# Optimization experiments

Hardware: AMD Instinct MI355X
Metric: run time of the kernel (lower is better)

## Reference

```python
import jax, jax.numpy as jnp
import numpy as np
from jax import lax

FEAT_STRIDE = 16
PRE_NMS_TOP_N = 6000   # cfg['TEST'].RPN_PRE_NMS_TOP_N
POST_NMS_TOP_N = 300   # cfg['TEST'].RPN_POST_NMS_TOP_N
NMS_THRESH = 0.7       # cfg['TEST'].RPN_NMS_THRESH
MIN_SIZE = 16.0        # cfg['TEST'].RPN_MIN_SIZE
B, A, H, W = 32, 9, 128, 128
NEG_INF = jnp.float32(-1e30)


def _whctrs(a):
    w = a[2] - a[0] + 1.0
    h = a[3] - a[1] + 1.0
    return w, h, a[0] + 0.5 * (w - 1), a[1] + 0.5 * (h - 1)

def _mkanchors(ws, hs, xc, yc):
    ws = ws[:, None]; hs = hs[:, None]
    return np.hstack((xc - 0.5 * (ws - 1), yc - 0.5 * (hs - 1),
                      xc + 0.5 * (ws - 1), yc + 0.5 * (hs - 1)))

def _ratio_enum(anchor, ratios):
    w, h, xc, yc = _whctrs(anchor)
    size = w * h
    ws = np.round(np.sqrt(size / ratios))
    hs = np.round(ws * ratios)
    return _mkanchors(ws, hs, xc, yc)

def _scale_enum(anchor, scales):
    w, h, xc, yc = _whctrs(anchor)
    return _mkanchors(w * scales, h * scales, xc, yc)

def generate_anchors(base_size=16, ratios=np.array([0.5, 1.0, 2.0]), scales=np.array([8.0, 16.0, 32.0])):
    base = np.array([1, 1, base_size, base_size], dtype=np.float64) - 1
    ra = _ratio_enum(base, ratios)
    return np.vstack([_scale_enum(ra[i], scales) for i in range(ra.shape[0])]).astype(np.float32)

_BASE_ANCHORS = generate_anchors()  # (A, 4)

def _all_anchors(h, w):
    sx = np.arange(w) * FEAT_STRIDE
    sy = np.arange(h) * FEAT_STRIDE
    sx, sy = np.meshgrid(sx, sy)  # row-major (h, w) matches permute(0,2,3,1) ordering
    shifts = np.stack([sx.ravel(), sy.ravel(), sx.ravel(), sy.ravel()], axis=1).astype(np.float32)
    return jnp.asarray((shifts[:, None, :] + _BASE_ANCHORS[None, :, :]).reshape(-1, 4))  # (h*w*A, 4)

# ---- bbox_transform_inv / clip_boxes ----

def _decode(anchors, deltas):
    ws = anchors[:, 2] - anchors[:, 0] + 1.0
    hs = anchors[:, 3] - anchors[:, 1] + 1.0
    cx = anchors[:, 0] + 0.5 * ws
    cy = anchors[:, 1] + 0.5 * hs
    dx, dy, dw, dh = deltas[:, 0], deltas[:, 1], deltas[:, 2], deltas[:, 3]
    pcx = dx * ws + cx
    pcy = dy * hs + cy
    pw = jnp.exp(dw) * ws
    ph = jnp.exp(dh) * hs
    return jnp.stack([pcx - 0.5 * pw, pcy - 0.5 * ph, pcx + 0.5 * pw, pcy + 0.5 * ph], axis=1)

def _clip(b, imh, imw):
    x1 = jnp.clip(b[:, 0], 0.0, imw - 1.0)
    y1 = jnp.clip(b[:, 1], 0.0, imh - 1.0)
    x2 = jnp.clip(b[:, 2], 0.0, imw - 1.0)
    y2 = jnp.clip(b[:, 3], 0.0, imh - 1.0)
    return jnp.stack([x1, y1, x2, y2], axis=1)

# ---- greedy NMS: pick top-score box, suppress IoU > thresh, repeat POST times ----

def _nms_select(boxes, scores):
    # boxes: (PRE, 4) score-sorted; scores: (PRE,)
    areas = (boxes[:, 2] - boxes[:, 0] + 1.0) * (boxes[:, 3] - boxes[:, 1] + 1.0)

    def body(i, st):
        s, keep, valid = st
        j = jnp.argmax(s)
        keep = keep.at[i].set(j)
        valid = valid.at[i].set(s[j] > NEG_INF)
        b = boxes[j]
        xx1 = jnp.maximum(b[0], boxes[:, 0])
        yy1 = jnp.maximum(b[1], boxes[:, 1])
        xx2 = jnp.minimum(b[2], boxes[:, 2])
        yy2 = jnp.minimum(b[3], boxes[:, 3])
        inter = jnp.maximum(xx2 - xx1 + 1.0, 0.0) * jnp.maximum(yy2 - yy1 + 1.0, 0.0)
        iou = inter / jnp.maximum(areas[j] + areas - inter, 1e-6)
        s = jnp.where(iou > NMS_THRESH, NEG_INF, s)  # suppresses j itself (IoU = 1)
        return s, keep, valid

    init = (scores, jnp.zeros((POST_NMS_TOP_N,), jnp.int32), jnp.zeros((POST_NMS_TOP_N,), bool))
    _, keep, valid = lax.fori_loop(0, POST_NMS_TOP_N, body, init)
    return keep, valid

def _per_image(sc, dl, info, anchors):
    prop = _clip(_decode(anchors, dl), info[0], info[1])  # (K*A, 4)
    ws = prop[:, 2] - prop[:, 0] + 1.0
    hs = prop[:, 3] - prop[:, 1] + 1.0
    min_sz = MIN_SIZE * info[2]
    sc = jnp.where((ws >= min_sz) & (hs >= min_sz), sc, NEG_INF)
    top_s, top_i = lax.top_k(sc, PRE_NMS_TOP_N)
    cand = prop[top_i]  # (PRE, 4)
    keep, valid = _nms_select(cand, top_s)
    return cand[keep] * valid[:, None].astype(cand.dtype)  # zero-pad invalid rows

def _forward(rpn_cls_prob, rpn_bbox_pred, im_info):
    b, _, h, w = rpn_cls_prob.shape
    anchors = _all_anchors(h, w)
    scores = rpn_cls_prob[:, A:, :, :].transpose(0, 2, 3, 1).reshape(b, -1)  # (b, h*w*A)
    deltas = rpn_bbox_pred.transpose(0, 2, 3, 1).reshape(b, -1, 4)           # (b, h*w*A, 4)
    boxes = jax.vmap(lambda s, d, i: _per_image(s, d, i, anchors))(scores, deltas, im_info)
    ids = jnp.broadcast_to(jnp.arange(b, dtype=boxes.dtype)[:, None, None], (b, POST_NMS_TOP_N, 1))
    return jnp.concatenate([ids, boxes], axis=2)  # (b, POST, 5): [batch_idx, x1, y1, x2, y2]

def setup_inputs() -> dict:
    key = jax.random.key(0)
    k1, k2 = jax.random.split(key)
    rpn_cls_prob = jax.random.uniform(k1, (B, 2 * A, H, W), dtype=jnp.float32)
    rpn_bbox_pred = jax.random.normal(k2, (B, 4 * A, H, W), dtype=jnp.float32) * 0.2
    im_info = jnp.tile(jnp.array([[H * FEAT_STRIDE, W * FEAT_STRIDE, 1.0]], dtype=jnp.float32), (B, 1))
    return {"rpn_cls_prob": rpn_cls_prob, "rpn_bbox_pred": rpn_bbox_pred, "im_info": im_info}

def reference(rpn_cls_prob, rpn_bbox_pred, im_info):
    return _forward(rpn_cls_prob, rpn_bbox_pred, im_info)
```

## Files before the change

kernel.cpp:

```cpp
#include <hip/hip_runtime.h>
#include <cstdint>
#include <cstddef>

#pragma clang fp contract(off)

typedef unsigned long long u64;

#define NB 32
#define NA 9
#define NH 128
#define NW 128
#define HW (NH*NW)
#define NANCH (NA*HW)
#define PRE_N 6000
#define POST_N 300
#define CAND_CAP 8192
#define NMS_T 0.7f
#define GX_GATHER 24
#define NBOX 6144
#define CH 512

__constant__ float c_wa[9] = {184.f,368.f,736.f,128.f,256.f,512.f,88.f,176.f,352.f};
__constant__ float c_ha[9] = {96.f,192.f,384.f,128.f,256.f,512.f,176.f,352.f,704.f};

__device__ __forceinline__ float4 decode_clip(int a, int h, int w,
    float dx, float dy, float dlw, float dlh, float imh, float imw) {
  float wa = c_wa[a], ha = c_ha[a];
  float cx = (float)w * 16.0f + 8.0f;
  float cy = (float)h * 16.0f + 8.0f;
  float pcx = dx * wa + cx;
  float pcy = dy * ha + cy;
  float pw = expf(dlw) * wa;
  float ph = expf(dlh) * ha;
  float x1 = pcx - 0.5f * pw;
  float y1 = pcy - 0.5f * ph;
  float x2 = pcx + 0.5f * pw;
  float y2 = pcy + 0.5f * ph;
  float4 r;
  r.x = fminf(fmaxf(x1, 0.0f), imw - 1.0f);
  r.y = fminf(fmaxf(y1, 0.0f), imh - 1.0f);
  r.z = fminf(fmaxf(x2, 0.0f), imw - 1.0f);
  r.w = fminf(fmaxf(y2, 0.0f), imh - 1.0f);
  return r;
}

__device__ __forceinline__ unsigned score_key(float sc, float bw, float bh, float msz) {
  unsigned bits = __float_as_uint(sc);
  unsigned key = (bits & 0x80000000u) ? ~bits : (bits | 0x80000000u);
  if (!(bw >= msz && bh >= msz)) key = 0u;
  return key;
}

__device__ __forceinline__ bool sup_test4(float4 v, float ar, float4 p, float pa) {
  float xx1 = fmaxf(p.x, v.x), yy1 = fmaxf(p.y, v.y);
  float xx2 = fminf(p.z, v.z), yy2 = fminf(p.w, v.w);
  float iw = fmaxf(xx2 - xx1 + 1.0f, 0.0f);
  float ih = fmaxf(yy2 - yy1 + 1.0f, 0.0f);
  float inter = iw * ih;
  float iou = inter / fmaxf(pa + ar - inter, 1e-6f);
  return iou > NMS_T;
}

__device__ __forceinline__ u64 shfl_xor_u64(u64 x, int m) {
  int lo = __shfl_xor((int)(unsigned)x, m, 64);
  int hi = __shfl_xor((int)(unsigned)(x >> 32), m, 64);
  return ((u64)(unsigned)hi << 32) | (unsigned)lo;
}

__device__ __forceinline__ void reg_step(u64 v[8], int t, int k, int j) {
  #pragma unroll
  for (int r = 0; r < 8; ++r) {
    if ((r & j) == 0) {
      int e = (t << 3) + r;
      bool up = ((e & k) == 0);
      u64 x = v[r], y = v[r | j];
      u64 mx = x > y ? x : y, mn = x > y ? y : x;
      v[r]     = up ? mx : mn;
      v[r | j] = up ? mn : mx;
    }
  }
}

__device__ __forceinline__ void shfl_step(u64 v[8], int t, int k, int j) {
  int m = j >> 3;
  bool lower = ((t & m) == 0);
  #pragma unroll
  for (int r = 0; r < 8; ++r) {
    int e = (t << 3) + r;
    bool up = ((e & k) == 0);
    u64 pv = shfl_xor_u64(v[r], m);
    bool keepmax = (up == lower);
    u64 x = v[r];
    u64 mx = x > pv ? x : pv, mn = x > pv ? pv : x;
    v[r] = keepmax ? mx : mn;
  }
}

__device__ __forceinline__ void lds_step(u64* sm, u64 v[8], int t, int k, int j) {
  int m = j >> 3;
  __syncthreads();
  #pragma unroll
  for (int r = 0; r < 8; ++r) sm[(r << 10) | t] = v[r];
  __syncthreads();
  bool lower = ((t & m) == 0);
  bool up = (((t << 3) & k) == 0);
  bool keepmax = (up == lower);
  int pt = t ^ m;
  #pragma unroll
  for (int r = 0; r < 8; ++r) {
    u64 pv = sm[(r << 10) | pt];
    u64 x = v[r];
    u64 mx = x > pv ? x : pv, mn = x > pv ? pv : x;
    v[r] = keepmax ? mx : mn;
  }
}

__device__ void find_B(const unsigned* __restrict__ hb, unsigned* part,
                       unsigned* outB, unsigned* outCum) {
  int tid = threadIdx.x;
  unsigned s = 0;
  for (int i = 0; i < 16; ++i) s += hb[tid*16 + i];
  part[tid] = s;
  __syncthreads();
  for (int off = 1; off < 256; off <<= 1) {
    unsigned v = (tid + off < 256) ? part[tid + off] : 0u;
    __syncthreads();
    part[tid] += v;
    __syncthreads();
  }
  unsigned St = part[tid];
  unsigned Sn = (tid < 255) ? part[tid + 1] : 0u;
  if (St >= (unsigned)PRE_N && Sn < (unsigned)PRE_N) {
    unsigned cum = Sn, B = 0, cumAbove = Sn;
    for (int i = 15; i >= 0; --i) {
      unsigned v = hb[tid*16 + i];
      if (cum + v >= (unsigned)PRE_N) { B = (unsigned)(tid*16 + i); cumAbove = cum; break; }
      cum += v;
    }
    *outB = B; *outCum = cumAbove;
  }
  __syncthreads();
}

__device__ void find_thr(const unsigned* __restrict__ hb2, unsigned B, unsigned cum0,
                         unsigned* part, unsigned* outThr) {
  int tid = threadIdx.x;
  unsigned s = 0;
  for (int i = 0; i < 16; ++i) s += hb2[tid*16 + i];
  part[tid] = s;
  __syncthreads();
  for (int off = 1; off < 256; off <<= 1) {
    unsigned v = (tid + off < 256) ? part[tid + off] : 0u;
    __syncthreads();
    part[tid] += v;
    __syncthreads();
  }
  unsigned St = cum0 + part[tid];
  unsigned Sn = cum0 + ((tid < 255) ? part[tid + 1] : 0u);
  if (St >= (unsigned)PRE_N && Sn < (unsigned)PRE_N) {
    unsigned cum = Sn, t = 1u;
    for (int i = 15; i >= 0; --i) {
      unsigned v = hb2[tid*16 + i];
      if (cum + v >= (unsigned)PRE_N) {
        t = (B << 20) | ((unsigned)(tid*16 + i) << 8);
        break;
      }
      cum += v;
    }
    if (t == 0u) t = 1u;
    *outThr = t;
  }
  __syncthreads();
}

__global__ __launch_bounds__(256) void k_keys(const float* __restrict__ cls,
    const float* __restrict__ dl, const float* __restrict__ info,
    unsigned* __restrict__ keys, unsigned* __restrict__ hist) {
  __shared__ unsigned hsh[4096];
  int tid = threadIdx.x;
  for (int i = tid; i < 4096; i += 256) hsh[i] = 0;
  int t = blockIdx.x * 256 + tid;
  int b = blockIdx.y;
  int hw0 = t * 4;
  int h = hw0 >> 7;
  const float* dlb  = dl  + (size_t)b * (4*NA*HW);
  const float* clsb = cls + (size_t)b * (2*NA*HW);
  float imh = info[b*3+0], imw = info[b*3+1];
  float msz = 16.0f * info[b*3+2];
  unsigned* kb = keys + (size_t)b * NANCH;
  __syncthreads();
  #pragma unroll
  for (int a = 0; a < 9; ++a) {
    float4 dx4 = *(const float4*)&dlb[(a*4+0)*HW + hw0];
    float4 dy4 = *(const float4*)&dlb[(a*4+1)*HW + hw0];
    float4 dw4 = *(const float4*)&dlb[(a*4+2)*HW + hw0];
    float4 dh4 = *(const float4*)&dlb[(a*4+3)*HW + hw0];
    float4 sc4 = *(const float4*)&clsb[(NA+a)*HW + hw0];
    uint4 out;
    {
      float4 bx = decode_clip(a, h, (hw0+0)&127, dx4.x, dy4.x, dw4.x, dh4.x, imh, imw);
      out.x = score_key(sc4.x, bx.z-bx.x+1.0f, bx.w-bx.y+1.0f, msz);
    }
    {
      float4 bx = decode_clip(a, h, (hw0+1)&127, dx4.y, dy4.y, dw4.y, dh4.y, imh, imw);
      out.y = score_key(sc4.y, bx.z-bx.x+1.0f, bx.w-bx.y+1.0f, msz);
    }
    {
      float4 bx = decode_clip(a, h, (hw0+2)&127, dx4.z, dy4.z, dw4.z, dh4.z, imh, imw);
      out.z = score_key(sc4.z, bx.z-bx.x+1.0f, bx.w-bx.y+1.0f, msz);
    }
    {
      float4 bx = decode_clip(a, h, (hw0+3)&127, dx4.w, dy4.w, dw4.w, dh4.w, imh, imw);
      out.w = score_key(sc4.w, bx.z-bx.x+1.0f, bx.w-bx.y+1.0f, msz);
    }
    *(uint4*)&kb[a*HW + hw0] = out;
    atomicAdd(&hsh[out.x >> 20], 1u);
    atomicAdd(&hsh[out.y >> 20], 1u);
    atomicAdd(&hsh[out.z >> 20], 1u);
    atomicAdd(&hsh[out.w >> 20], 1u);
  }
  __syncthreads();
  unsigned* gb = hist + ((size_t)b << 12);
  for (int i = tid; i < 4096; i += 256) {
    unsigned v = hsh[i];
    if (v) atomicAdd(&gb[i], v);
  }
}

__global__ __launch_bounds__(256) void k_hist2(const unsigned* __restrict__ keys,
    const unsigned* __restrict__ hist1, unsigned* __restrict__ hist2) {
  __shared__ unsigned h[4096];
  __shared__ unsigned part[256];
  __shared__ unsigned sB, sCum;
  int b = blockIdx.y, tid = threadIdx.x;
  for (int i = tid; i < 4096; i += 256) h[i] = 0;
  __syncthreads();
  find_B(hist1 + ((size_t)b << 12), part, &sB, &sCum);
  unsigned B = sB;
  const unsigned* kb = keys + (size_t)b * NANCH;
  for (int i = blockIdx.x * 256 + tid; i < NANCH; i += gridDim.x * 256) {
    unsigned k = kb[i];
    if ((k >> 20) == B) atomicAdd(&h[(k >> 8) & 4095u], 1u);
  }
  __syncthreads();
  unsigned* gb = hist2 + ((size_t)b << 12);
  for (int i = tid; i < 4096; i += 256) { unsigned v = h[i]; if (v) atomicAdd(&gb[i], v); }
}

__global__ __launch_bounds__(256) void k_gather(const unsigned* __restrict__ keys,
    const unsigned* __restrict__ hist1, const unsigned* __restrict__ hist2,
    const float* __restrict__ dl, const float* __restrict__ info,
    unsigned* __restrict__ cnt, u64* __restrict__ cand,
    float4* __restrict__ boxes) {
  int b = blockIdx.y, tid = threadIdx.x;
  int lane = tid & 63, wv = tid >> 6;
  __shared__ unsigned part[256];
  __shared__ unsigned sB, sCum, sThr;
  __shared__ unsigned wcnt[4], woff[4], blkbase;
  if (tid == 0) sThr = 1u;
  __syncthreads();
  find_B(hist1 + ((size_t)b << 12), part, &sB, &sCum);
  find_thr(hist2 + ((size_t)b << 12), sB, sCum, part, &sThr);
  unsigned t_ = sThr;
  const unsigned* kb = keys + (size_t)b * NANCH;
  const float* dlb = dl + (size_t)b * (4*NA*HW);
  float imh = info[b*3+0], imw = info[b*3+1];
  u64* cb = cand + (size_t)b * CAND_CAP;
  float4* bxc = boxes + (size_t)b * CAND_CAP;
  unsigned* cp = cnt + (size_t)b * 64;
  const int PER_BLK = NANCH / GX_GATHER;
  int base0 = blockIdx.x * PER_BLK;
  for (int it = 0; it < PER_BLK / 256; ++it) {
    int j = base0 + it * 256 + tid;
    unsigned key = kb[j];
    bool pass = key >= t_;
    u64 mask = __ballot(pass);
    if (lane == 0) wcnt[wv] = (unsigned)__popcll(mask);
    __syncthreads();
    if (tid == 0) {
      unsigned s0 = 0;
      for (int w = 0; w < 4; ++w) { woff[w] = s0; s0 += wcnt[w]; }
      blkbase = s0 ? atomicAdd(cp, s0) : 0u;
    }
    __syncthreads();
    if (pass) {
      unsigned pos = blkbase + woff[wv] + (unsigned)__popcll(mask & ((1ull << lane) - 1ull));
      if (pos < CAND_CAP) {
        int a = j >> 14, hw = j & (HW - 1);
        unsigned oi = (unsigned)(hw * 9 + a);
        unsigned noi = (~oi) & 0x3FFFFu;
        cb[pos] = ((u64)key << 32) | ((u64)noi << 13) | (u64)pos;
        bxc[pos] = decode_clip(a, hw >> 7, hw & 127,
                               dlb[(a*4+0)*HW + hw], dlb[(a*4+1)*HW + hw],
                               dlb[(a*4+2)*HW + hw], dlb[(a*4+3)*HW + hw],
                               imh, imw);
      }
    }
    __syncthreads();
  }
}

__global__ __launch_bounds__(1024) void k_final4(const u64* __restrict__ cand,
    const unsigned* __restrict__ cnt, const float4* __restrict__ boxes,
    float* __restrict__ out) {
  __shared__ float4 bx[NBOX];
  __shared__ float4 cbox2[CH];
  __shared__ float  carea2[CH];
  __shared__ float4 kbox[POST_N];
  __shared__ float  karea[POST_N];
  __shared__ unsigned supf[CH];
  __shared__ u64 sup[CH][9];
  __shared__ u64 aliveM[8];
  __shared__ u64 kgW[8];
  __shared__ int s_nk;
  u64* sm = (u64*)bx;

  int b = blockIdx.x, tid = threadIdx.x;
  int lane = tid & 63;
  if (tid == 0) s_nk = 0;

  unsigned effcnt = cnt[b * 64];
  if (effcnt > CAND_CAP) effcnt = CAND_CAP;
  const u64* cb = cand + (size_t)b * CAND_CAP;
  int e0 = tid << 3;
  u64 v[8];
  #pragma unroll
  for (int r = 0; r < 8; ++r)
    v[r] = ((unsigned)(e0 + r) < effcnt) ? cb[e0 + r] : 0ull;

  for (int k = 2; k <= 8; k <<= 1)
    for (int j = k >> 1; j >= 1; j >>= 1) reg_step(v, tid, k, j);
  for (int k = 16; k <= CAND_CAP; k <<= 1) {
    int j = k >> 1;
    for (; j >= 512; j >>= 1) lds_step(sm, v, tid, k, j);
    for (; j >= 8;   j >>= 1) shfl_step(v, tid, k, j);
    for (; j >= 1;   j >>= 1) reg_step(v, tid, k, j);
  }
  __syncthreads();

  const float4* bxc = boxes + (size_t)b * CAND_CAP;
  #pragma unroll
  for (int r = 0; r < 8; ++r) {
    int rank = e0 + r;
    if (rank < NBOX) {
      u64 ck = (rank < PRE_N) ? v[r] : 0ull;
      float4 w = make_float4(0.f, 0.f, -1.f, -1.f);
      if ((unsigned)(ck >> 32) != 0u)
        w = bxc[(unsigned)(ck & 0x1FFFu)];
      bx[rank] = w;
    }
  }
  __syncthreads();

  float* ob = out + (size_t)b * (POST_N * 5);
  int c = tid & (CH - 1);
  int seg = tid >> 9;

  for (int base = 0; base < NBOX; base += CH) {
    if (tid < CH) {
      float4 w = bx[base + tid];
      supf[tid] = (w.z - w.x + 1.0f > 0.0f) ? 0u : 1u;
    }
    __syncthreads();
    int nk0 = s_nk;

    if (supf[c] == 0u && nk0 > 0) {
      float4 w = bx[base + c];
      float ar = (w.z - w.x + 1.0f) * (w.w - w.y + 1.0f);
      bool dead = false;
      for (int k = seg; k < nk0; k += 2) {
        if (sup_test4(w, ar, kbox[k], karea[k])) { dead = true; break; }
      }
      if (dead) supf[c] = 1u;
    }
    __syncthreads();

    if (tid < CH) {
      u64 am = __ballot(supf[tid] == 0u);
      if (lane == 0) aliveM[tid >> 6] = am;
    }
    __syncthreads();

    int na = 0;
    #pragma unroll
    for (int g = 0; g < 8; ++g) na += (int)__popcll(aliveM[g]);
    if (na == 0) continue;

    if (tid < CH && supf[tid] == 0u) {
      int cg2 = tid >> 6;
      int pre = 0;
      #pragma unroll
      for (int g = 0; g < 8; ++g) if (g < cg2) pre += (int)__popcll(aliveM[g]);
      pre += (int)__popcll(aliveM[cg2] & ((1ull << (tid & 63)) - 1ull));
      float4 w = bx[base + tid];
      cbox2[pre] = w;
      carea2[pre] = (w.z - w.x + 1.0f) * (w.w - w.y + 1.0f);
    }
    __syncthreads();

    {
      int i = c;
      if (i < na) {
        int ngi = (i >> 6) + 1;
        int gA = seg ? (ngi >> 1) : 0;
        int gB = seg ? ngi : (ngi >> 1);
        if (gA < gB) {
          float4 vi = cbox2[i];
          float ai = carea2[i];
          for (int g = gA; g < gB; ++g) {
            int jmax = i - (g << 6);
            if (jmax > 64) jmax = 64;
            u64 r = 0;
            #pragma unroll 4
            for (int j = 0; j < jmax; ++j) {
              if (sup_test4(vi, ai, cbox2[(g << 6) + j], carea2[(g << 6) + j]))
                r |= 1ull << j;
            }
            sup[i][g] = r;
          }
        }
      }
    }
    __syncthreads();

    if (tid < 64) {
      u64 kw[8];
      #pragma unroll
      for (int s = 0; s < 8; ++s) {
        u64 kg = 0;
        if (s * 64 < na) {
          int cc = s * 64 + lane;
          bool a = (cc < na);
          #pragma unroll
          for (int g = 0; g < 8; ++g) {
            if (g < s && a) a = (sup[cc][g] & kw[g]) == 0ull;
          }
          u64 r = a ? sup[cc][s] : 0ull;
          u64 cm = __ballot(a);
          while (cm) {
            int j = __builtin_ctzll(cm);
            kg |= 1ull << j;
            u64 rem = __ballot((r >> j) & 1ull);
            cm &= ~(rem | (1ull << j));
          }
        }
        kw[s] = kg;
      }
      if (lane == 0) {
        #pragma unroll
        for (int s = 0; s < 8; ++s) kgW[s] = kw[s];
      }
    }
    __syncthreads();

    if (tid < na) {
      int s = tid >> 6;
      u64 kgw = kgW[s];
      bool kept = (kgw >> (tid & 63)) & 1;
      int pre = 0;
      #pragma unroll
      for (int g = 0; g < 8; ++g) if (g < s) pre += (int)__popcll(kgW[g]);
      pre += (int)__popcll(kgw & ((1ull << (tid & 63)) - 1ull));
      int rank = nk0 + pre;
      if (kept && rank < POST_N) {
        float4 w = cbox2[tid];
        kbox[rank] = w; karea[rank] = carea2[tid];
        ob[rank*5+0] = (float)b;
        ob[rank*5+1] = w.x; ob[rank*5+2] = w.y; ob[rank*5+3] = w.z; ob[rank*5+4] = w.w;
      }
    }
    if (tid == 0) {
      int tot = 0;
      #pragma unroll
      for (int s = 0; s < 8; ++s) tot += (int)__popcll(kgW[s]);
      int nn = nk0 + tot;
      s_nk = nn < POST_N ? nn : POST_N;
    }
    __syncthreads();
    if (s_nk >= POST_N) break;
  }
  __syncthreads();
  int nk = s_nk;
  for (int r = nk + tid; r < POST_N; r += 1024) {
    ob[r*5+0] = (float)b;
    ob[r*5+1] = 0.f; ob[r*5+2] = 0.f; ob[r*5+3] = 0.f; ob[r*5+4] = 0.f;
  }
}

extern "C" void kernel_launch(void* const* d_in, const int* in_sizes, int n_in,
                              void* d_out, int out_size, void* d_ws, size_t ws_size,
                              hipStream_t stream) {
  const float* cls  = (const float*)d_in[0];
  const float* dl   = (const float*)d_in[1];
  const float* info = (const float*)d_in[2];
  float* out = (float*)d_out;
  char* ws = (char*)d_ws;

  const size_t OFF_KEYS = 0;
  const size_t OFF_H1   = 18874368;
  const size_t OFF_H2   = 19398656;
  const size_t OFF_CNT  = 19922944;
  const size_t OFF_CAND = 19931136;
  const size_t OFF_BOX  = 22028288;
  const size_t WS_NEED  = 26222592;
  if (ws_size < WS_NEED) return;

  unsigned* keys  = (unsigned*)(ws + OFF_KEYS);
  unsigned* h1    = (unsigned*)(ws + OFF_H1);
  unsigned* h2    = (unsigned*)(ws + OFF_H2);
  unsigned* cnt   = (unsigned*)(ws + OFF_CNT);
  u64* cand = (u64*)(ws + OFF_CAND);
  float4* boxes = (float4*)(ws + OFF_BOX);

  hipMemsetAsync(ws + OFF_H1, 0, OFF_CAND - OFF_H1, stream);

  dim3 g1(HW / 1024, NB);
  k_keys<<<g1, 256, 0, stream>>>(cls, dl, info, keys, h1);
  dim3 gh(8, NB);
  k_hist2<<<gh, 256, 0, stream>>>(keys, h1, h2);
  dim3 gg(GX_GATHER, NB);
  k_gather<<<gg, 256, 0, stream>>>(keys, h1, h2, dl, info, cnt, cand, boxes);
  k_final4<<<NB, 1024, 0, stream>>>(cand, cnt, boxes, out);
}
```

Baseline: 332.4 us.

## Fuse second-level histogram and gather into one per-image select kernel

Merges k_hist2 and k_gather into a single 1024-thread block per image. The block builds the refinement histogram in shared memory, computes the threshold locally, and compacts candidates with a two-pass count-then-write scheme using per-wave offsets, which removes the global atomics and the per-iteration block barriers. The NMS keep-scan in k_final4 now prefetches the suppression rows into registers. This cuts a kernel launch and a memset range but reduces parallelism to 32 blocks for the key scans, which each read the key array twice.

```diff
diff --git a/kernel.cpp b/kernel.cpp
--- a/kernel.cpp
+++ b/kernel.cpp
@@ -16,7 +16,6 @@
 #define POST_N 300
 #define CAND_CAP 8192
 #define NMS_T 0.7f
-#define GX_GATHER 24
 #define NBOX 6144
 #define CH 512
 
@@ -118,26 +117,31 @@
 __device__ void find_B(const unsigned* __restrict__ hb, unsigned* part,
                        unsigned* outB, unsigned* outCum) {
   int tid = threadIdx.x;
-  unsigned s = 0;
-  for (int i = 0; i < 16; ++i) s += hb[tid*16 + i];
-  part[tid] = s;
+  if (tid < 256) {
+    unsigned s = 0;
+    for (int i = 0; i < 16; ++i) s += hb[tid*16 + i];
+    part[tid] = s;
+  }
   __syncthreads();
   for (int off = 1; off < 256; off <<= 1) {
-    unsigned v = (tid + off < 256) ? part[tid + off] : 0u;
-    __syncthreads();
-    part[tid] += v;
-    __syncthreads();
-  }
-  unsigned St = part[tid];
-  unsigned Sn = (tid < 255) ? part[tid + 1] : 0u;
-  if (St >= (unsigned)PRE_N && Sn < (unsigned)PRE_N) {
-    unsigned cum = Sn, B = 0, cumAbove = Sn;
-    for (int i = 15; i >= 0; --i) {
-      unsigned v = hb[tid*16 + i];
-      if (cum + v >= (unsigned)PRE_N) { B = (unsigned)(tid*16 + i); cumAbove = cum; break; }
-      cum += v;
-    }
-    *outB = B; *outCum = cumAbove;
+    unsigned v = 0;
+    if (tid < 256 && tid + off < 256) v = part[tid + off];
+    __syncthreads();
+    if (tid < 256) part[tid] += v;
+    __syncthreads();
+  }
+  if (tid < 256) {
+    unsigned St = part[tid];
+    unsigned Sn = (tid < 255) ? part[tid + 1] : 0u;
+    if (St >= (unsigned)PRE_N && Sn < (unsigned)PRE_N) {
+      unsigned cum = Sn, B = 0, cumAbove = Sn;
+      for (int i = 15; i >= 0; --i) {
+        unsigned v = hb[tid*16 + i];
+        if (cum + v >= (unsigned)PRE_N) { B = (unsigned)(tid*16 + i); cumAbove = cum; break; }
+        cum += v;
+      }
+      *outB = B; *outCum = cumAbove;
+    }
   }
   __syncthreads();
 }
@@ -145,30 +149,35 @@
 __device__ void find_thr(const unsigned* __restrict__ hb2, unsigned B, unsigned cum0,
                          unsigned* part, unsigned* outThr) {
   int tid = threadIdx.x;
-  unsigned s = 0;
-  for (int i = 0; i < 16; ++i) s += hb2[tid*16 + i];
-  part[tid] = s;
+  if (tid < 256) {
+    unsigned s = 0;
+    for (int i = 0; i < 16; ++i) s += hb2[tid*16 + i];
+    part[tid] = s;
+  }
   __syncthreads();
   for (int off = 1; off < 256; off <<= 1) {
-    unsigned v = (tid + off < 256) ? part[tid + off] : 0u;
-    __syncthreads();
-    part[tid] += v;
-    __syncthreads();
-  }
-  unsigned St = cum0 + part[tid];
-  unsigned Sn = cum0 + ((tid < 255) ? part[tid + 1] : 0u);
-  if (St >= (unsigned)PRE_N && Sn < (unsigned)PRE_N) {
-    unsigned cum = Sn, t = 1u;
-    for (int i = 15; i >= 0; --i) {
-      unsigned v = hb2[tid*16 + i];
-      if (cum + v >= (unsigned)PRE_N) {
-        t = (B << 20) | ((unsigned)(tid*16 + i) << 8);
-        break;
-      }
-      cum += v;
-    }
-    if (t == 0u) t = 1u;
-    *outThr = t;
+    unsigned v = 0;
+    if (tid < 256 && tid + off < 256) v = part[tid + off];
+    __syncthreads();
+    if (tid < 256) part[tid] += v;
+    __syncthreads();
+  }
+  if (tid < 256) {
+    unsigned St = cum0 + part[tid];
+    unsigned Sn = cum0 + ((tid < 255) ? part[tid + 1] : 0u);
+    if (St >= (unsigned)PRE_N && Sn < (unsigned)PRE_N) {
+      unsigned cum = Sn, t = 1u;
+      for (int i = 15; i >= 0; --i) {
+        unsigned v = hb2[tid*16 + i];
+        if (cum + v >= (unsigned)PRE_N) {
+          t = (B << 20) | ((unsigned)(tid*16 + i) << 8);
+          break;
+        }
+        cum += v;
+      }
+      if (t == 0u) t = 1u;
+      *outThr = t;
+    }
   }
   __syncthreads();
 }
@@ -227,76 +236,96 @@
   }
 }
 
-__global__ __launch_bounds__(256) void k_hist2(const unsigned* __restrict__ keys,
-    const unsigned* __restrict__ hist1, unsigned* __restrict__ hist2) {
-  __shared__ unsigned h[4096];
-  __shared__ unsigned part[256];
-  __shared__ unsigned sB, sCum;
-  int b = blockIdx.y, tid = threadIdx.x;
-  for (int i = tid; i < 4096; i += 256) h[i] = 0;
-  __syncthreads();
-  find_B(hist1 + ((size_t)b << 12), part, &sB, &sCum);
-  unsigned B = sB;
-  const unsigned* kb = keys + (size_t)b * NANCH;
-  for (int i = blockIdx.x * 256 + tid; i < NANCH; i += gridDim.x * 256) {
-    unsigned k = kb[i];
-    if ((k >> 20) == B) atomicAdd(&h[(k >> 8) & 4095u], 1u);
-  }
-  __syncthreads();
-  unsigned* gb = hist2 + ((size_t)b << 12);
-  for (int i = tid; i < 4096; i += 256) { unsigned v = h[i]; if (v) atomicAdd(&gb[i], v); }
-}
-
-__global__ __launch_bounds__(256) void k_gather(const unsigned* __restrict__ keys,
-    const unsigned* __restrict__ hist1, const unsigned* __restrict__ hist2,
+__global__ __launch_bounds__(1024) void k_select(
+    const unsigned* __restrict__ keys, const unsigned* __restrict__ hist1,
     const float* __restrict__ dl, const float* __restrict__ info,
     unsigned* __restrict__ cnt, u64* __restrict__ cand,
     float4* __restrict__ boxes) {
-  int b = blockIdx.y, tid = threadIdx.x;
-  int lane = tid & 63, wv = tid >> 6;
+  __shared__ unsigned h[4096];
   __shared__ unsigned part[256];
   __shared__ unsigned sB, sCum, sThr;
-  __shared__ unsigned wcnt[4], woff[4], blkbase;
+  __shared__ unsigned wcnt[16], woff[16];
+  int b = blockIdx.x, tid = threadIdx.x;
+  int lane = tid & 63, wv = tid >> 6;
+
+  for (int i = tid; i < 4096; i += 1024) h[i] = 0u;
   if (tid == 0) sThr = 1u;
   __syncthreads();
+
   find_B(hist1 + ((size_t)b << 12), part, &sB, &sCum);
-  find_thr(hist2 + ((size_t)b << 12), sB, sCum, part, &sThr);
+  unsigned B = sB;
+
+  const unsigned* kb = keys + (size_t)b * NANCH;
+  const uint4* kb4 = (const uint4*)kb;
+  for (int i = tid; i < NANCH/4; i += 1024) {
+    uint4 kk = kb4[i];
+    if ((kk.x >> 20) == B) atomicAdd(&h[(kk.x >> 8) & 4095u], 1u);
+    if ((kk.y >> 20) == B) atomicAdd(&h[(kk.y >> 8) & 4095u], 1u);
+    if ((kk.z >> 20) == B) atomicAdd(&h[(kk.z >> 8) & 4095u], 1u);
+    if ((kk.w >> 20) == B) atomicAdd(&h[(kk.w >> 8) & 4095u], 1u);
+  }
+  __syncthreads();
+  find_thr(h, B, sCum, part, &sThr);
   unsigned t_ = sThr;
-  const unsigned* kb = keys + (size_t)b * NANCH;
+
+  const int PW = NANCH / 16;
+  int base_w = wv * PW;
+  unsigned wtot = 0;
+  for (int it = 0; it < PW / 128; ++it) {
+    int j0 = base_w + it * 128 + lane * 2;
+    uint2 kk = *(const uint2*)&kb[j0];
+    u64 m0 = __ballot(kk.x >= t_), m1 = __ballot(kk.y >= t_);
+    wtot += (unsigned)(__popcll(m0) + __popcll(m1));
+  }
+  if (lane == 0) wcnt[wv] = wtot;
+  __syncthreads();
+  if (tid == 0) {
+    unsigned s0 = 0;
+    for (int w = 0; w < 16; ++w) { woff[w] = s0; s0 += wcnt[w]; }
+    cnt[b * 64] = s0;
+  }
+  __syncthreads();
+
   const float* dlb = dl + (size_t)b * (4*NA*HW);
   float imh = info[b*3+0], imw = info[b*3+1];
   u64* cb = cand + (size_t)b * CAND_CAP;
   float4* bxc = boxes + (size_t)b * CAND_CAP;
-  unsigned* cp = cnt + (size_t)b * 64;
-  const int PER_BLK = NANCH / GX_GATHER;
-  int base0 = blockIdx.x * PER_BLK;
-  for (int it = 0; it < PER_BLK / 256; ++it) {
-    int j = base0 + it * 256 + tid;
-    unsigned key = kb[j];
-    bool pass = key >= t_;
-    u64 mask = __ballot(pass);
-    if (lane == 0) wcnt[wv] = (unsigned)__popcll(mask);
-    __syncthreads();
-    if (tid == 0) {
-      unsigned s0 = 0;
-      for (int w = 0; w < 4; ++w) { woff[w] = s0; s0 += wcnt[w]; }
-      blkbase = s0 ? atomicAdd(cp, s0) : 0u;
-    }
-    __syncthreads();
-    if (pass) {
-      unsigned pos = blkbase + woff[wv] + (unsigned)__popcll(mask & ((1ull << lane) - 1ull));
+  unsigned wpos = woff[wv];
+  u64 lt = (1ull << lane) - 1ull;
+  for (int it = 0; it < PW / 128; ++it) {
+    int j0 = base_w + it * 128 + lane * 2;
+    uint2 kk = *(const uint2*)&kb[j0];
+    bool p0 = kk.x >= t_, p1 = kk.y >= t_;
+    u64 m0 = __ballot(p0), m1 = __ballot(p1);
+    if (p0) {
+      unsigned pos = wpos + (unsigned)__popcll(m0 & lt);
       if (pos < CAND_CAP) {
+        int j = j0;
         int a = j >> 14, hw = j & (HW - 1);
         unsigned oi = (unsigned)(hw * 9 + a);
         unsigned noi = (~oi) & 0x3FFFFu;
-        cb[pos] = ((u64)key << 32) | ((u64)noi << 13) | (u64)pos;
+        cb[pos] = ((u64)kk.x << 32) | ((u64)noi << 13) | (u64)pos;
         bxc[pos] = decode_clip(a, hw >> 7, hw & 127,
                                dlb[(a*4+0)*HW + hw], dlb[(a*4+1)*HW + hw],
                                dlb[(a*4+2)*HW + hw], dlb[(a*4+3)*HW + hw],
                                imh, imw);
       }
     }
-    __syncthreads();
+    if (p1) {
+      unsigned pos = wpos + (unsigned)__popcll(m0) + (unsigned)__popcll(m1 & lt);
+      if (pos < CAND_CAP) {
+        int j = j0 + 1;
+        int a = j >> 14, hw = j & (HW - 1);
+        unsigned oi = (unsigned)(hw * 9 + a);
+        unsigned noi = (~oi) & 0x3FFFFu;
+        cb[pos] = ((u64)kk.y << 32) | ((u64)noi << 13) | (u64)pos;
+        bxc[pos] = decode_clip(a, hw >> 7, hw & 127,
+                               dlb[(a*4+0)*HW + hw], dlb[(a*4+1)*HW + hw],
+                               dlb[(a*4+2)*HW + hw], dlb[(a*4+3)*HW + hw],
+                               imh, imw);
+      }
+    }
+    wpos += (unsigned)(__popcll(m0) + __popcll(m1));
   }
 }
 
@@ -425,17 +454,31 @@
 
     if (tid < 64) {
       u64 kw[8];
+      int nst = (na + 63) >> 6;
+      u64 srow[8];
+      {
+        const u64* rp = sup[lane];
+        #pragma unroll
+        for (int g = 0; g < 8; ++g) srow[g] = rp[g];
+      }
       #pragma unroll
       for (int s = 0; s < 8; ++s) {
+        u64 nsr[8];
+        bool pf = (s + 1 < nst);
+        if (pf) {
+          const u64* rp = sup[(s + 1) * 64 + lane];
+          #pragma unroll
+          for (int g = 0; g < 8; ++g) nsr[g] = rp[g];
+        }
         u64 kg = 0;
-        if (s * 64 < na) {
+        if (s < nst) {
           int cc = s * 64 + lane;
           bool a = (cc < na);
+          u64 blocked = 0;
           #pragma unroll
-          for (int g = 0; g < 8; ++g) {
-            if (g < s && a) a = (sup[cc][g] & kw[g]) == 0ull;
-          }
-          u64 r = a ? sup[cc][s] : 0ull;
+          for (int g = 0; g < 8; ++g) if (g < s) blocked |= (srow[g] & kw[g]);
+          a = a && (blocked == 0ull);
+          u64 r = a ? srow[s] : 0ull;
           u64 cm = __ballot(a);
           while (cm) {
             int j = __builtin_ctzll(cm);
@@ -445,6 +488,10 @@
           }
         }
         kw[s] = kg;
+        if (pf) {
+          #pragma unroll
+          for (int g = 0; g < 8; ++g) srow[g] = nsr[g];
+        }
       }
       if (lane == 0) {
         #pragma unroll
@@ -504,21 +551,18 @@
   const size_t OFF_BOX  = 22028288;
   const size_t WS_NEED  = 26222592;
   if (ws_size < WS_NEED) return;
+  (void)OFF_H2;
 
   unsigned* keys  = (unsigned*)(ws + OFF_KEYS);
   unsigned* h1    = (unsigned*)(ws + OFF_H1);
-  unsigned* h2    = (unsigned*)(ws + OFF_H2);
   unsigned* cnt   = (unsigned*)(ws + OFF_CNT);
   u64* cand = (u64*)(ws + OFF_CAND);
   float4* boxes = (float4*)(ws + OFF_BOX);
 
-  hipMemsetAsync(ws + OFF_H1, 0, OFF_CAND - OFF_H1, stream);
+  hipMemsetAsync(ws + OFF_H1, 0, 524288, stream);
 
   dim3 g1(HW / 1024, NB);
   k_keys<<<g1, 256, 0, stream>>>(cls, dl, info, keys, h1);
-  dim3 gh(8, NB);
-  k_hist2<<<gh, 256, 0, stream>>>(keys, h1, h2);
-  dim3 gg(GX_GATHER, NB);
-  k_gather<<<gg, 256, 0, stream>>>(keys, h1, h2, dl, info, cnt, cand, boxes);
+  k_select<<<NB, 1024, 0, stream>>>(keys, h1, dl, info, cnt, cand, boxes);
   k_final4<<<NB, 1024, 0, stream>>>(cand, cnt, boxes, out);
 }
```

Result: slower. 393.6 us (+18.4%).
